# Kernel tuning notes

Measured on AMD Instinct MI355X. Metric: run time of the kernel, lower is better.

Reference implementation:

```python
import jax, jax.numpy as jnp
import numpy as np

B, L, M = 2, 1024, 32
F_DIM, C_DIM = 256, 32
H, QK = 12, 16
INF = 100000.0
EPS_DIR = 1e-4
LN_EPS = 1e-5
BETA_COEF = float(np.sqrt(2.0 / 9.0) / 2.0)
LOGIT_SCALE = float(np.sqrt(1.0 / 3.0))


def gather_nodes(a, nb):
    # a: (B,L,...,D), nb: (B,L,M) -> (B,L,M,...,D); row m of query l is node nb[b,l,m]
    return jax.vmap(lambda ab, nbb: ab[nbb])(a, nb)


def gather_pairs(z, nb):
    # z: (B,L,L,C), nb: (B,L,M) -> (B,L,M,C)
    idx = jnp.broadcast_to(nb[..., None], nb.shape + (z.shape[-1],))
    return jnp.take_along_axis(z, idx, axis=2)


def setup_inputs() -> dict:
    key = jax.random.key(0)
    ks = jax.random.split(key, 12)
    inp = {
        'R': jax.random.normal(ks[0], (B, L, 3, 3), jnp.float32),
        't': jax.random.normal(ks[1], (B, L, 3), jnp.float32),
        'p_CB': jax.random.normal(ks[2], (B, L, 3), jnp.float32),
        'x': jax.random.normal(ks[3], (B, L, F_DIM), jnp.float32),
        'z': jax.random.normal(ks[4], (B, L, L, C_DIM), jnp.float32),
        'mask': jnp.ones((B, L), dtype=bool),
        'neighbors': jax.random.randint(ks[5], (B, L, M), 0, L),
        'Wq': jax.random.normal(ks[6], (F_DIM, H * QK), jnp.float32) * 0.05,
        'Wk': jax.random.normal(ks[7], (F_DIM, H * QK), jnp.float32) * 0.05,
        'Wv': jax.random.normal(ks[8], (F_DIM, H * QK), jnp.float32) * 0.05,
        'Wpair': jax.random.normal(ks[9], (C_DIM, H), jnp.float32) * 0.1,
        'spatial_coef': jnp.full((1, 1, 1, H), float(np.log(np.e - 1.0)), jnp.float32),
        'Wout': jax.random.normal(ks[10], (H * C_DIM + H * QK + 7 * H, F_DIM), jnp.float32) * 0.05,
        'b_out': jnp.zeros((F_DIM,), jnp.float32),
        'ln_gamma': jnp.ones((F_DIM,), jnp.float32),
        'ln_beta': jnp.zeros((F_DIM,), jnp.float32),
    }
    return inp


def reference(R, t, p_CB, x, z, mask, neighbors, Wq, Wk, Wv, Wpair,
              spatial_coef, Wout, b_out, ln_gamma, ln_beta):
    Bn, Ln, Fn = x.shape
    # pair features of each query's KNN neighbors
    z_knn = gather_pairs(z, neighbors)                      # (B,L,M,C)
    # node logits
    q = (x @ Wq).reshape(Bn, Ln, H, QK)
    k = (x @ Wk).reshape(Bn, Ln, H, QK)
    k_knn = gather_nodes(k, neighbors)                      # (B,L,M,H,QK)
    logits_node = jnp.einsum('blhd,blmhd->blmh', q, k_knn)
    # pair bias logits
    logits_pair = z_knn @ Wpair                             # (B,L,M,H)
    # spatial (beta-carbon distance) logits; identical across heads before gamma
    p_knn = gather_nodes(p_CB, neighbors)                   # (B,L,M,3)
    d2 = jnp.sum((p_CB[:, :, None, :] - p_knn) ** 2, axis=-1)  # (B,L,M)
    gamma = jax.nn.softplus(spatial_coef)                   # (1,1,1,H)
    logits_spatial = d2[..., None] * (-gamma * BETA_COEF)   # (B,L,M,H)
    logits = (logits_node + logits_pair + logits_spatial) * LOGIT_SCALE
    # row-mask + softmax over neighbor dim
    mask_row = mask[:, :, None, None]                       # (B,L,1,1)
    logits = jnp.where(mask_row, logits, logits - INF)
    alpha = jax.nn.softmax(logits, axis=2)
    alpha = jnp.where(mask_row, alpha, jnp.zeros_like(alpha))
    # aggregations
    feat_p2n = jnp.einsum('blmh,blmc->blhc', alpha, z_knn).reshape(Bn, Ln, -1)
    v = (x @ Wv).reshape(Bn, Ln, H, QK)
    v_knn = gather_nodes(v, neighbors)                      # (B,L,M,H,QK)
    feat_node = jnp.einsum('blmh,blmhd->blhd', alpha, v_knn).reshape(Bn, Ln, -1)
    aggr = jnp.einsum('blmh,blmi->blhi', alpha, p_knn)      # (B,L,H,3) global coords
    # global_to_local: R^T (q - t)
    local = jnp.einsum('blji,blhj->blhi', R, aggr - t[:, :, None, :])
    dist = jnp.linalg.norm(local, axis=-1)                  # (B,L,H)
    dirn = local / (jnp.linalg.norm(local, axis=-1, keepdims=True) + EPS_DIR)
    feat_spatial = jnp.concatenate([local.reshape(Bn, Ln, -1), dist,
                                    dirn.reshape(Bn, Ln, -1)], axis=-1)
    feat = jnp.concatenate([feat_p2n, feat_node, feat_spatial], axis=-1)
    out = feat @ Wout + b_out
    out = jnp.where(mask[:, :, None], out, jnp.zeros_like(out))
    h = x + out
    mu = jnp.mean(h, axis=-1, keepdims=True)
    var = jnp.var(h, axis=-1, keepdims=True)
    return (h - mu) / jnp.sqrt(var + LN_EPS) * ln_gamma + ln_beta
```

## Files before the change

### kernel.cpp

```cpp
#include <hip/hip_runtime.h>
#include <math.h>

#define B_   2
#define L_   1024
#define M_   32
#define F_   256
#define C_   32
#define H_   12
#define QK_  16
#define HQK  192
#define KV2  384
#define QKV3 576
#define FEAT 660
#define FPAD 672
#define A2S  1360
#define NTOK 2048

constexpr float EPS_DIR     = 1e-4f;
constexpr float LN_EPS      = 1e-5f;
constexpr float BETA_COEF   = 0.23570226039551585f;
constexpr float LOGIT_SCALE = 0.5773502691896258f;

typedef __attribute__((ext_vector_type(8))) short  bf16x8;
typedef __attribute__((ext_vector_type(4))) float  f32x4;
typedef __attribute__((ext_vector_type(8))) ushort u16x8;

static __device__ __forceinline__ ushort f2bf(float v) {
  union { float f; unsigned u; } x; x.f = v;
  unsigned r = x.u + 0x7FFFu + ((x.u >> 16) & 1u);
  return (ushort)(r >> 16);
}
static __device__ __forceinline__ float bf2f(ushort h) {
  union { float f; unsigned u; } x; x.u = ((unsigned)h) << 16;
  return x.f;
}
static __device__ __forceinline__ void split4(const float* v,
                                              ushort4& h, ushort4& l) {
  h.x = f2bf(v[0]); l.x = f2bf(v[0] - bf2f(h.x));
  h.y = f2bf(v[1]); l.y = f2bf(v[1] - bf2f(h.y));
  h.z = f2bf(v[2]); l.z = f2bf(v[2] - bf2f(h.z));
  h.w = f2bf(v[3]); l.w = f2bf(v[3] - bf2f(h.w));
}
static __device__ __forceinline__ ushort4 pack4(const float* v) {
  ushort4 h;
  h.x = f2bf(v[0]); h.y = f2bf(v[1]);
  h.z = f2bf(v[2]); h.w = f2bf(v[3]);
  return h;
}
static __device__ __forceinline__ void wave_sync() {
  asm volatile("s_waitcnt lgkmcnt(0)" ::: "memory");
}

__global__ __launch_bounds__(256) void qkv_prep_kernel(
    const float* __restrict__ x,
    const float* __restrict__ Wq, const float* __restrict__ Wk,
    const float* __restrict__ Wv, const float* __restrict__ Wout,
    const float* __restrict__ z, const int* __restrict__ neighbors,
    float* __restrict__ qf, ushort* __restrict__ kvb,
    ushort* __restrict__ wo,
    ushort* __restrict__ z_d) {
  __shared__ ushort Ah[64][36], Al[64][36];
  __shared__ ushort Bh[64][36];
  const int bx  = blockIdx.x;
  const int tid = threadIdx.x;

  if (bx < 512) {
    const int t0 = bx * 4;
    for (int i = tid; i < 1024; i += 256) {
      int t = i >> 8, r = i & 255, m = r >> 3, cq = r & 7;
      int tok = t0 + t;
      int nb  = neighbors[tok * M_ + m];
      float4 v = *(const float4*)&z[((size_t)tok * L_ + nb) * C_ + cq * 4];
      *(ushort4*)&z_d[((size_t)tok * M_ + m) * C_ + cq * 4] =
          pack4((const float*)&v);
    }
    return;
  }
  if (bx < 544) {
    const int base = (bx - 512) * 256 + tid;
#pragma unroll
    for (int rep = 0; rep < 6; ++rep) {
      int qid = base + rep * 8192;
      if (qid < 43008) {
        int col = qid / 168;
        int k   = (qid - col * 168) * 4;
        float v[4];
#pragma unroll
        for (int j = 0; j < 4; ++j)
          v[j] = (k + j < FEAT) ? Wout[(size_t)(k + j) * F_ + col] : 0.f;
        ushort4 h4 = pack4(v);
        int off = (k >> 5) * 32 + ((k & 16) >> 4) * 4 + ((k & 12) << 1);
        *(ushort4*)&wo[(size_t)col * FPAD + off] = h4;
      }
    }
    return;
  }

  const int bxm = bx - 544;
  const int t0  = (bxm & 31) * 64;
  const int c0  = (bxm >> 5) * 64;
  const int w   = tid >> 6;
  const int l   = tid & 63;
  const int lr  = l & 15;
  const int lk  = (l >> 4) * 4;

  const float* Wb   = (c0 < HQK) ? Wq : (c0 < 2 * HQK) ? Wk : Wv;
  const int    cOff = (c0 < HQK) ? c0 : (c0 < 2 * HQK) ? c0 - HQK
                                                       : c0 - 2 * HQK;

  union ABFrag { bf16x8 v; ushort4 h[2]; };

  const int arow0 = tid >> 3,  akc0 = (tid & 7) * 4;
  const int arow1 = (tid + 256) >> 3, akc1 = ((tid + 256) & 7) * 4;
  const int bk0 = tid >> 4,  bcc0 = (tid & 15) * 4;
  const int bk1 = (tid + 256) >> 4, bcc1 = ((tid + 256) & 15) * 4;

  f32x4 acc[4];
#pragma unroll
  for (int n = 0; n < 4; ++n) acc[n] = (f32x4){0.f, 0.f, 0.f, 0.f};

  float4 xr0 = *(const float4*)&x[(size_t)(t0 + arow0) * F_ + akc0];
  float4 xr1 = *(const float4*)&x[(size_t)(t0 + arow1) * F_ + akc1];
  float4 wr0 = *(const float4*)&Wb[(size_t)bk0 * HQK + cOff + bcc0];
  float4 wr1 = *(const float4*)&Wb[(size_t)bk1 * HQK + cOff + bcc1];

  for (int s = 0; s < 8; ++s) {
    __syncthreads();
    {
      ushort4 h4, l4;
      split4((const float*)&xr0, h4, l4);
      *(ushort4*)&Ah[arow0][akc0] = h4;
      *(ushort4*)&Al[arow0][akc0] = l4;
      split4((const float*)&xr1, h4, l4);
      *(ushort4*)&Ah[arow1][akc1] = h4;
      *(ushort4*)&Al[arow1][akc1] = l4;
      ushort4 b0 = pack4((const float*)&wr0);
      Bh[bcc0 + 0][bk0] = b0.x;  Bh[bcc0 + 1][bk0] = b0.y;
      Bh[bcc0 + 2][bk0] = b0.z;  Bh[bcc0 + 3][bk0] = b0.w;
      ushort4 b1 = pack4((const float*)&wr1);
      Bh[bcc1 + 0][bk1] = b1.x;  Bh[bcc1 + 1][bk1] = b1.y;
      Bh[bcc1 + 2][bk1] = b1.z;  Bh[bcc1 + 3][bk1] = b1.w;
    }
    __syncthreads();

    if (s < 7) {
      int sn = (s + 1) * 32;
      xr0 = *(const float4*)&x[(size_t)(t0 + arow0) * F_ + sn + akc0];
      xr1 = *(const float4*)&x[(size_t)(t0 + arow1) * F_ + sn + akc1];
      wr0 = *(const float4*)&Wb[(size_t)(sn + bk0) * HQK + cOff + bcc0];
      wr1 = *(const float4*)&Wb[(size_t)(sn + bk1) * HQK + cOff + bcc1];
    }

    ABFrag a_h, a_l;
    a_h.h[0] = *(const ushort4*)&Ah[w * 16 + lr][lk];
    a_h.h[1] = *(const ushort4*)&Ah[w * 16 + lr][16 + lk];
    a_l.h[0] = *(const ushort4*)&Al[w * 16 + lr][lk];
    a_l.h[1] = *(const ushort4*)&Al[w * 16 + lr][16 + lk];
#pragma unroll
    for (int n = 0; n < 4; ++n) {
      ABFrag b_h;
      b_h.h[0] = *(const ushort4*)&Bh[n * 16 + lr][lk];
      b_h.h[1] = *(const ushort4*)&Bh[n * 16 + lr][16 + lk];
      acc[n] = __builtin_amdgcn_mfma_f32_16x16x32_bf16(a_h.v, b_h.v, acc[n], 0, 0, 0);
      acc[n] = __builtin_amdgcn_mfma_f32_16x16x32_bf16(a_l.v, b_h.v, acc[n], 0, 0, 0);
    }
  }

  if (c0 < HQK) {
#pragma unroll
    for (int n = 0; n < 4; ++n)
#pragma unroll
      for (int i = 0; i < 4; ++i)
        qf[(size_t)(t0 + w * 16 + lk + i) * HQK + c0 + n * 16 + lr] =
            acc[n][i];
  } else {
    const int cb0 = c0 - HQK;
#pragma unroll
    for (int n = 0; n < 4; ++n)
#pragma unroll
      for (int i = 0; i < 4; ++i)
        kvb[(size_t)(t0 + w * 16 + lk + i) * KV2 + cb0 + n * 16 + lr] =
            f2bf(acc[n][i]);
  }
}

__global__ __launch_bounds__(512) void attn_out_kernel(
    const float* __restrict__ R, const float* __restrict__ tvec,
    const float* __restrict__ pCB, const ushort* __restrict__ z_d,
    const int*   __restrict__ neighbors,
    const float* __restrict__ Wpair, const float* __restrict__ spatial_coef,
    const float* __restrict__ qf, const ushort* __restrict__ kvb,
    const ushort* __restrict__ wo,
    const float* __restrict__ b_out, const float* __restrict__ x,
    const float* __restrict__ ln_g, const float* __restrict__ ln_b,
    float* __restrict__ out) {
  const int tid   = threadIdx.x;
  const int t0    = blockIdx.x * 8;
  const int bbase = t0 & ~(L_ - 1);

  __shared__ float  q_s[8][HQK];
  __shared__ ushort z_s[8][M_][36];
  __shared__ float  alpha_s[8][M_][13];
  __shared__ float  p_s[8][M_][4];
  __shared__ float  wp_s[C_ * H_];
  __shared__ float  gam_s[H_];
  __shared__ float  geo_s[8][16];
  __shared__ int    nb_s[8][M_];
  __shared__ float  aggr_s[8][H_][4];
  __shared__ ushort A2[8][A2S];
  __shared__ float  part[16][8][2];
  __shared__ float  mu_s[16], rs_s[16];

  if (tid < 256) {
    int t = tid >> 5, m = tid & 31;
    nb_s[t][m] = neighbors[(t0 + t) * M_ + m];
  } else if (tid - 256 < H_) {
    gam_s[tid - 256] = log1pf(expf(spatial_coef[tid - 256]));
  }
  if (tid < C_ * H_) wp_s[tid] = Wpair[tid];
  if (tid < 96) {
    int t = tid / 12, c = FEAT + tid % 12;
    A2[t][(c >> 2) * 8 + (c & 3)]     = 0;
    A2[t][(c >> 2) * 8 + (c & 3) + 4] = 0;
  }
  if (tid < 384) {
    int t = tid / 48, r = tid % 48;
    *(float4*)&q_s[t][r * 4] =
        *(const float4*)&qf[(size_t)(t0 + t) * HQK + r * 4];
  }
  if (tid >= 384 && tid < 504) {
    int j = tid - 384, t = j / 15, w = j % 15;
    geo_s[t][w] = (w < 3) ? pCB[(t0 + t) * 3 + w]
                : (w < 6) ? tvec[(t0 + t) * 3 + (w - 3)]
                          : R[(t0 + t) * 9 + (w - 6)];
  }
  for (int i = tid; i < 2048; i += 512) {
    int t = i >> 8, r = i & 255, m = r >> 3, cq = r & 7;
    ushort4 v = *(const ushort4*)&z_d[((size_t)(t0 + t) * M_ + m) * C_ + cq * 4];
    *(ushort4*)&z_s[t][m][cq * 4] = v;
  }
  for (int i = tid; i < 8 * M_ * 3; i += 512) {
    int t = i / 96, r = i % 96, m = r / 3, ii = r % 3;
    int nb = neighbors[(t0 + t) * M_ + m];
    p_s[t][m][ii] = pCB[(bbase + nb) * 3 + ii];
  }
  __syncthreads();

  const int wv = tid >> 6;
  const int l  = tid & 63;

  {
    const int t  = wv;
    const int m  = l & 31;
    const int hb = (l >> 5) * 6;
    const int nb = nb_s[t][m];
    float lg[6];
#pragma unroll
    for (int h = 0; h < 6; ++h) lg[h] = 0.f;
#pragma unroll
    for (int c = 0; c < C_; ++c) {
      float zv = bf2f(z_s[t][m][c]);
#pragma unroll
      for (int h = 0; h < 6; ++h) lg[h] += zv * wp_s[c * H_ + hb + h];
    }
    union U8 { u16x8 v; ushort e[8]; };
    const ushort* kr = kvb + (size_t)(bbase + nb) * KV2;
#pragma unroll
    for (int h = 0; h < 6; ++h) {
      const int hh = hb + h;
      U8 ka, kb2;
      ka.v  = *(const u16x8*)&kr[hh * 16];
      kb2.v = *(const u16x8*)&kr[hh * 16 + 8];
      const float4* q4 = (const float4*)&q_s[t][hh * 16];
      float4 qa = q4[0], qb = q4[1], qc = q4[2], qd = q4[3];
      float nd = bf2f(ka.e[0]) * qa.x + bf2f(ka.e[1]) * qa.y
               + bf2f(ka.e[2]) * qa.z + bf2f(ka.e[3]) * qa.w
               + bf2f(ka.e[4]) * qb.x + bf2f(ka.e[5]) * qb.y
               + bf2f(ka.e[6]) * qb.z + bf2f(ka.e[7]) * qb.w
               + bf2f(kb2.e[0]) * qc.x + bf2f(kb2.e[1]) * qc.y
               + bf2f(kb2.e[2]) * qc.z + bf2f(kb2.e[3]) * qc.w
               + bf2f(kb2.e[4]) * qd.x + bf2f(kb2.e[5]) * qd.y
               + bf2f(kb2.e[6]) * qd.z + bf2f(kb2.e[7]) * qd.w;
      lg[h] += nd;
    }
    float dx = geo_s[t][0] - p_s[t][m][0];
    float dy = geo_s[t][1] - p_s[t][m][1];
    float dz = geo_s[t][2] - p_s[t][m][2];
    float d2 = dx * dx + dy * dy + dz * dz;
#pragma unroll
    for (int h = 0; h < 6; ++h)
      lg[h] = (lg[h] - d2 * gam_s[hb + h] * BETA_COEF) * LOGIT_SCALE;
#pragma unroll
    for (int h = 0; h < 6; ++h) {
      float mx = lg[h];
#pragma unroll
      for (int o = 16; o; o >>= 1) mx = fmaxf(mx, __shfl_xor(mx, o));
      float p = expf(lg[h] - mx);
      float s = p;
#pragma unroll
      for (int o = 16; o; o >>= 1) s += __shfl_xor(s, o);
      alpha_s[t][m][hb + h] = p / s;
    }
  }
  wave_sync();

  {
    const int t = wv;
    const int hp = l >> 3, cq = l & 7;
    if (hp < 6) {
      float acc0[4] = {0, 0, 0, 0}, acc1[4] = {0, 0, 0, 0};
#pragma unroll
      for (int m = 0; m < M_; ++m) {
        float a0 = alpha_s[t][m][hp * 2];
        float a1 = alpha_s[t][m][hp * 2 + 1];
        ushort4 zz = *(const ushort4*)&z_s[t][m][cq * 4];
        float z0 = bf2f(zz.x), z1 = bf2f(zz.y);
        float z2 = bf2f(zz.z), z3 = bf2f(zz.w);
        acc0[0] += a0 * z0; acc0[1] += a0 * z1;
        acc0[2] += a0 * z2; acc0[3] += a0 * z3;
        acc1[0] += a1 * z0; acc1[1] += a1 * z1;
        acc1[2] += a1 * z2; acc1[3] += a1 * z3;
      }
      ushort4 h4, l4;
      int c = (hp * 2) * C_ + cq * 4;
      split4(acc0, h4, l4);
      *(ushort4*)&A2[t][c * 2]     = h4;
      *(ushort4*)&A2[t][c * 2 + 4] = l4;
      c = (hp * 2 + 1) * C_ + cq * 4;
      split4(acc1, h4, l4);
      *(ushort4*)&A2[t][c * 2]     = h4;
      *(ushort4*)&A2[t][c * 2 + 4] = l4;
    }
  }
  {
    const int t = wv;
    const int h = l >> 2, dq = l & 3;
    if (h < 12) {
      float acc[4] = {0, 0, 0, 0};
#pragma unroll
      for (int m = 0; m < M_; ++m) {
        float a = alpha_s[t][m][h];
        const ushort* vr = kvb + (size_t)(bbase + nb_s[t][m]) * KV2 + HQK;
        ushort4 v4 = *(const ushort4*)&vr[h * QK_ + dq * 4];
        acc[0] += a * bf2f(v4.x); acc[1] += a * bf2f(v4.y);
        acc[2] += a * bf2f(v4.z); acc[3] += a * bf2f(v4.w);
      }
      ushort4 h4, l4;
      split4(acc, h4, l4);
      int c = 384 + h * QK_ + dq * 4;
      *(ushort4*)&A2[t][c * 2]     = h4;
      *(ushort4*)&A2[t][c * 2 + 4] = l4;
    }
  }
  if (l < 36) {
    const int t = wv;
    int h = l / 3, ii = l % 3;
    float f = 0.f;
#pragma unroll
    for (int m = 0; m < M_; ++m) f += alpha_s[t][m][h] * p_s[t][m][ii];
    aggr_s[t][h][ii] = f;
  }
  wave_sync();

  if (l < 12) {
    const int t = wv;
    const int h = l;
    float a0 = aggr_s[t][h][0] - geo_s[t][3];
    float a1 = aggr_s[t][h][1] - geo_s[t][4];
    float a2 = aggr_s[t][h][2] - geo_s[t][5];
    float lx = geo_s[t][6] * a0 + geo_s[t][9]  * a1 + geo_s[t][12] * a2;
    float ly = geo_s[t][7] * a0 + geo_s[t][10] * a1 + geo_s[t][13] * a2;
    float lz = geo_s[t][8] * a0 + geo_s[t][11] * a1 + geo_s[t][14] * a2;
    float dist = sqrtf(lx * lx + ly * ly + lz * lz);
    float inv  = 1.f / (dist + EPS_DIR);
    float vals[7] = {lx, ly, lz, dist, lx * inv, ly * inv, lz * inv};
    int   cols[7] = {576 + 3 * h, 577 + 3 * h, 578 + 3 * h, 612 + h,
                     624 + 3 * h, 625 + 3 * h, 626 + 3 * h};
#pragma unroll
    for (int j = 0; j < 7; ++j) {
      int c = cols[j];
      ushort hh = f2bf(vals[j]);
      A2[t][(c >> 2) * 8 + (c & 3)]     = hh;
      A2[t][(c >> 2) * 8 + (c & 3) + 4] = f2bf(vals[j] - bf2f(hh));
    }
  }

  const int w  = wv;
  const int lr = l & 15, lk = (l >> 4) * 4;
  const int atok = lr & 7;
  const int asel = (lr >> 3) * 4;
  const int col0 = (w * 2 + 0) * 16 + lr;
  const int col1 = (w * 2 + 1) * 16 + lr;
  const ushort* wo0 = wo + (size_t)col0 * FPAD + lk * 2;
  const ushort* wo1 = wo + (size_t)col1 * FPAD + lk * 2;

  union ABFrag { bf16x8 v; ushort4 h[2]; };
  union B8 { u16x8 v; ushort4 q[2]; };

  B8 pb[4][2];

#define PREF_B(sstep, buf) do {                                          \
    pb[buf][0].v = *(const u16x8*)&wo0[(sstep) * 32];                    \
    pb[buf][1].v = *(const u16x8*)&wo1[(sstep) * 32];                    \
  } while (0)

  PREF_B(0, 0);
  PREF_B(1, 1);
  PREF_B(2, 2);
  PREF_B(3, 3);
  __syncthreads();

  f32x4 acc[2];
  acc[0] = (f32x4){0.f, 0.f, 0.f, 0.f};
  acc[1] = (f32x4){0.f, 0.f, 0.f, 0.f};

#pragma unroll
  for (int s = 0; s < 21; ++s) {
    const int cb = s & 3;
    const int k0 = s * 32 + lk;
    ABFrag a;
    a.h[0] = *(const ushort4*)&A2[atok][k0 * 2 + asel];
    a.h[1] = *(const ushort4*)&A2[atok][(k0 + 16) * 2 + asel];
    ABFrag b0, b1;
    b0.h[0] = pb[cb][0].q[0];  b0.h[1] = pb[cb][0].q[1];
    b1.h[0] = pb[cb][1].q[0];  b1.h[1] = pb[cb][1].q[1];
    if (s < 17) PREF_B(s + 4, cb);
    acc[0] = __builtin_amdgcn_mfma_f32_16x16x32_bf16(a.v, b0.v, acc[0], 0, 0, 0);
    acc[1] = __builtin_amdgcn_mfma_f32_16x16x32_bf16(a.v, b1.v, acc[1], 0, 0, 0);
  }
#undef PREF_B

#pragma unroll
  for (int n = 0; n < 2; ++n)
#pragma unroll
    for (int i = 0; i < 4; ++i)
      acc[n][i] += __shfl_xor(acc[n][i], 32);

  float hv[4][2];
#pragma unroll
  for (int i = 0; i < 4; ++i) {
    const int row = (lk + i) & 7;
#pragma unroll
    for (int n = 0; n < 2; ++n) {
      const int col = (w * 2 + n) * 16 + lr;
      hv[i][n] = acc[n][i] + b_out[col] + x[(size_t)(t0 + row) * F_ + col];
    }
  }
#pragma unroll
  for (int i = 0; i < 4; ++i) {
    float s  = hv[i][0] + hv[i][1];
    float sq = hv[i][0] * hv[i][0] + hv[i][1] * hv[i][1];
#pragma unroll
    for (int o = 1; o < 16; o <<= 1) {
      s  += __shfl_xor(s, o);
      sq += __shfl_xor(sq, o);
    }
    if (lr == 0) {
      part[lk + i][w][0] = s;
      part[lk + i][w][1] = sq;
    }
  }
  __syncthreads();
  if (tid < 16) {
    float s = 0.f, sq = 0.f;
#pragma unroll
    for (int ww = 0; ww < 8; ++ww) {
      s  += part[tid][ww][0];
      sq += part[tid][ww][1];
    }
    float mu = s * (1.f / F_);
    mu_s[tid] = mu;
    rs_s[tid] = rsqrtf(sq * (1.f / F_) - mu * mu + LN_EPS);
  }
  __syncthreads();

  if (lk < 8) {
#pragma unroll
    for (int n = 0; n < 2; ++n) {
      const int col = (w * 2 + n) * 16 + lr;
      const float g = ln_g[col], be = ln_b[col];
#pragma unroll
      for (int i = 0; i < 4; ++i) {
        const int row = lk + i;
        out[(size_t)(t0 + row) * F_ + col] =
            (hv[i][n] - mu_s[row]) * rs_s[row] * g + be;
      }
    }
  }
}

extern "C" void kernel_launch(void* const* d_in, const int* in_sizes, int n_in,
                              void* d_out, int out_size, void* d_ws,
                              size_t ws_size, hipStream_t stream) {
  const float* R     = (const float*)d_in[0];
  const float* t     = (const float*)d_in[1];
  const float* pCB   = (const float*)d_in[2];
  const float* x     = (const float*)d_in[3];
  const float* z     = (const float*)d_in[4];
  const int*   nb    = (const int*)d_in[6];
  const float* Wq    = (const float*)d_in[7];
  const float* Wk    = (const float*)d_in[8];
  const float* Wv    = (const float*)d_in[9];
  const float* Wpair = (const float*)d_in[10];
  const float* sc    = (const float*)d_in[11];
  const float* Wout  = (const float*)d_in[12];
  const float* bout  = (const float*)d_in[13];
  const float* g     = (const float*)d_in[14];
  const float* be    = (const float*)d_in[15];
  float* out  = (float*)d_out;

  float*  qf   = (float*)d_ws;
  ushort* kvb  = (ushort*)(qf + (size_t)NTOK * HQK);
  ushort* z_d  = kvb + (size_t)NTOK * KV2;
  ushort* wo   = z_d + (size_t)NTOK * M_ * C_;

  qkv_prep_kernel<<<832, 256, 0, stream>>>(x, Wq, Wk, Wv, Wout, z, nb,
                                           qf, kvb, wo, z_d);
  attn_out_kernel<<<NTOK / 8, 512, 0, stream>>>(R, t, pCB, z_d, nb, Wpair,
                                                sc, qf, kvb, wo, bout, x,
                                                g, be, out);
}
```

Before: 37.58 us.

## Halve attn_out block to 256 threads with two tokens and four column tiles per wave

The attention/output kernel drops from 8 waves to 4 waves per block. Each wave now handles two tokens in the softmax and aggregation phases, and four 16-column output tiles in the MFMA projection. The prefetch depth for Wout drops from 4 stages to 2, while each stage loads four fragments. The intent is to reuse each A fragment across more MFMAs and to cut per-block synchronisation and launch cost. The trade-offs are higher register pressure, more serial work per wave and lower latency hiding.

Measured after the change: 47.07 us. +25.3%, slower.

```diff
diff --git a/kernel.cpp b/kernel.cpp
--- a/kernel.cpp
+++ b/kernel.cpp
@@ -184,7 +184,7 @@
   }
 }
 
-__global__ __launch_bounds__(512) void attn_out_kernel(
+__global__ __launch_bounds__(256) void attn_out_kernel(
     const float* __restrict__ R, const float* __restrict__ tvec,
     const float* __restrict__ pCB, const ushort* __restrict__ z_d,
     const int*   __restrict__ neighbors,
@@ -208,38 +208,37 @@
   __shared__ int    nb_s[8][M_];
   __shared__ float  aggr_s[8][H_][4];
   __shared__ ushort A2[8][A2S];
-  __shared__ float  part[16][8][2];
+  __shared__ float  part[16][4][2];
   __shared__ float  mu_s[16], rs_s[16];
 
-  if (tid < 256) {
+  {
     int t = tid >> 5, m = tid & 31;
     nb_s[t][m] = neighbors[(t0 + t) * M_ + m];
-  } else if (tid - 256 < H_) {
-    gam_s[tid - 256] = log1pf(expf(spatial_coef[tid - 256]));
-  }
-  if (tid < C_ * H_) wp_s[tid] = Wpair[tid];
+  }
+  if (tid < H_) gam_s[tid] = log1pf(expf(spatial_coef[tid]));
+  for (int i = tid; i < C_ * H_; i += 256) wp_s[i] = Wpair[i];
   if (tid < 96) {
     int t = tid / 12, c = FEAT + tid % 12;
     A2[t][(c >> 2) * 8 + (c & 3)]     = 0;
     A2[t][(c >> 2) * 8 + (c & 3) + 4] = 0;
   }
-  if (tid < 384) {
-    int t = tid / 48, r = tid % 48;
+  for (int i = tid; i < 384; i += 256) {
+    int t = i / 48, r = i % 48;
     *(float4*)&q_s[t][r * 4] =
         *(const float4*)&qf[(size_t)(t0 + t) * HQK + r * 4];
   }
-  if (tid >= 384 && tid < 504) {
-    int j = tid - 384, t = j / 15, w = j % 15;
+  if (tid >= 128 && tid < 248) {
+    int j = tid - 128, t = j / 15, w = j % 15;
     geo_s[t][w] = (w < 3) ? pCB[(t0 + t) * 3 + w]
                 : (w < 6) ? tvec[(t0 + t) * 3 + (w - 3)]
                           : R[(t0 + t) * 9 + (w - 6)];
   }
-  for (int i = tid; i < 2048; i += 512) {
+  for (int i = tid; i < 2048; i += 256) {
     int t = i >> 8, r = i & 255, m = r >> 3, cq = r & 7;
     ushort4 v = *(const ushort4*)&z_d[((size_t)(t0 + t) * M_ + m) * C_ + cq * 4];
     *(ushort4*)&z_s[t][m][cq * 4] = v;
   }
-  for (int i = tid; i < 8 * M_ * 3; i += 512) {
+  for (int i = tid; i < 8 * M_ * 3; i += 256) {
     int t = i / 96, r = i % 96, m = r / 3, ii = r % 3;
     int nb = neighbors[(t0 + t) * M_ + m];
     p_s[t][m][ii] = pCB[(bbase + nb) * 3 + ii];
@@ -249,8 +248,8 @@
   const int wv = tid >> 6;
   const int l  = tid & 63;
 
-  {
-    const int t  = wv;
+  for (int tt = 0; tt < 2; ++tt) {
+    const int t  = wv * 2 + tt;
     const int m  = l & 31;
     const int hb = (l >> 5) * 6;
     const int nb = nb_s[t][m];
@@ -304,8 +303,8 @@
   }
   wave_sync();
 
-  {
-    const int t = wv;
+  for (int tt = 0; tt < 2; ++tt) {
+    const int t = wv * 2 + tt;
     const int hp = l >> 3, cq = l & 7;
     if (hp < 6) {
       float acc0[4] = {0, 0, 0, 0}, acc1[4] = {0, 0, 0, 0};
@@ -332,8 +331,8 @@
       *(ushort4*)&A2[t][c * 2 + 4] = l4;
     }
   }
-  {
-    const int t = wv;
+  for (int tt = 0; tt < 2; ++tt) {
+    const int t = wv * 2 + tt;
     const int h = l >> 2, dq = l & 3;
     if (h < 12) {
       float acc[4] = {0, 0, 0, 0};
@@ -352,119 +351,130 @@
       *(ushort4*)&A2[t][c * 2 + 4] = l4;
     }
   }
-  if (l < 36) {
-    const int t = wv;
-    int h = l / 3, ii = l % 3;
-    float f = 0.f;
-#pragma unroll
-    for (int m = 0; m < M_; ++m) f += alpha_s[t][m][h] * p_s[t][m][ii];
-    aggr_s[t][h][ii] = f;
+  for (int tt = 0; tt < 2; ++tt) {
+    const int t = wv * 2 + tt;
+    if (l < 36) {
+      int h = l / 3, ii = l % 3;
+      float f = 0.f;
+#pragma unroll
+      for (int m = 0; m < M_; ++m) f += alpha_s[t][m][h] * p_s[t][m][ii];
+      aggr_s[t][h][ii] = f;
+    }
   }
   wave_sync();
 
-  if (l < 12) {
-    const int t = wv;
-    const int h = l;
-    float a0 = aggr_s[t][h][0] - geo_s[t][3];
-    float a1 = aggr_s[t][h][1] - geo_s[t][4];
-    float a2 = aggr_s[t][h][2] - geo_s[t][5];
-    float lx = geo_s[t][6] * a0 + geo_s[t][9]  * a1 + geo_s[t][12] * a2;
-    float ly = geo_s[t][7] * a0 + geo_s[t][10] * a1 + geo_s[t][13] * a2;
-    float lz = geo_s[t][8] * a0 + geo_s[t][11] * a1 + geo_s[t][14] * a2;
-    float dist = sqrtf(lx * lx + ly * ly + lz * lz);
-    float inv  = 1.f / (dist + EPS_DIR);
-    float vals[7] = {lx, ly, lz, dist, lx * inv, ly * inv, lz * inv};
-    int   cols[7] = {576 + 3 * h, 577 + 3 * h, 578 + 3 * h, 612 + h,
-                     624 + 3 * h, 625 + 3 * h, 626 + 3 * h};
-#pragma unroll
-    for (int j = 0; j < 7; ++j) {
-      int c = cols[j];
-      ushort hh = f2bf(vals[j]);
-      A2[t][(c >> 2) * 8 + (c & 3)]     = hh;
-      A2[t][(c >> 2) * 8 + (c & 3) + 4] = f2bf(vals[j] - bf2f(hh));
-    }
-  }
-
-  const int w  = wv;
+  for (int tt = 0; tt < 2; ++tt) {
+    const int t = wv * 2 + tt;
+    if (l < 12) {
+      const int h = l;
+      float a0 = aggr_s[t][h][0] - geo_s[t][3];
+      float a1 = aggr_s[t][h][1] - geo_s[t][4];
+      float a2 = aggr_s[t][h][2] - geo_s[t][5];
+      float lx = geo_s[t][6] * a0 + geo_s[t][9]  * a1 + geo_s[t][12] * a2;
+      float ly = geo_s[t][7] * a0 + geo_s[t][10] * a1 + geo_s[t][13] * a2;
+      float lz = geo_s[t][8] * a0 + geo_s[t][11] * a1 + geo_s[t][14] * a2;
+      float dist = sqrtf(lx * lx + ly * ly + lz * lz);
+      float inv  = 1.f / (dist + EPS_DIR);
+      float vals[7] = {lx, ly, lz, dist, lx * inv, ly * inv, lz * inv};
+      int   cols[7] = {576 + 3 * h, 577 + 3 * h, 578 + 3 * h, 612 + h,
+                       624 + 3 * h, 625 + 3 * h, 626 + 3 * h};
+#pragma unroll
+      for (int j = 0; j < 7; ++j) {
+        int c = cols[j];
+        ushort hh = f2bf(vals[j]);
+        A2[t][(c >> 2) * 8 + (c & 3)]     = hh;
+        A2[t][(c >> 2) * 8 + (c & 3) + 4] = f2bf(vals[j] - bf2f(hh));
+      }
+    }
+  }
+
   const int lr = l & 15, lk = (l >> 4) * 4;
   const int atok = lr & 7;
   const int asel = (lr >> 3) * 4;
-  const int col0 = (w * 2 + 0) * 16 + lr;
-  const int col1 = (w * 2 + 1) * 16 + lr;
-  const ushort* wo0 = wo + (size_t)col0 * FPAD + lk * 2;
-  const ushort* wo1 = wo + (size_t)col1 * FPAD + lk * 2;
+  int colv[4];
+  const ushort* wop[4];
+#pragma unroll
+  for (int n = 0; n < 4; ++n) {
+    colv[n] = (wv * 4 + n) * 16 + lr;
+    wop[n]  = wo + (size_t)colv[n] * FPAD + lk * 2;
+  }
 
   union ABFrag { bf16x8 v; ushort4 h[2]; };
   union B8 { u16x8 v; ushort4 q[2]; };
 
-  B8 pb[4][2];
+  B8 pb[2][4];
 
 #define PREF_B(sstep, buf) do {                                          \
-    pb[buf][0].v = *(const u16x8*)&wo0[(sstep) * 32];                    \
-    pb[buf][1].v = *(const u16x8*)&wo1[(sstep) * 32];                    \
+    pb[buf][0].v = *(const u16x8*)&wop[0][(sstep) * 32];                 \
+    pb[buf][1].v = *(const u16x8*)&wop[1][(sstep) * 32];                 \
+    pb[buf][2].v = *(const u16x8*)&wop[2][(sstep) * 32];                 \
+    pb[buf][3].v = *(const u16x8*)&wop[3][(sstep) * 32];                 \
   } while (0)
 
   PREF_B(0, 0);
   PREF_B(1, 1);
-  PREF_B(2, 2);
-  PREF_B(3, 3);
   __syncthreads();
 
-  f32x4 acc[2];
-  acc[0] = (f32x4){0.f, 0.f, 0.f, 0.f};
-  acc[1] = (f32x4){0.f, 0.f, 0.f, 0.f};
+  f32x4 acc[4];
+#pragma unroll
+  for (int n = 0; n < 4; ++n) acc[n] = (f32x4){0.f, 0.f, 0.f, 0.f};
 
 #pragma unroll
   for (int s = 0; s < 21; ++s) {
-    const int cb = s & 3;
+    const int cb = s & 1;
     const int k0 = s * 32 + lk;
     ABFrag a;
     a.h[0] = *(const ushort4*)&A2[atok][k0 * 2 + asel];
     a.h[1] = *(const ushort4*)&A2[atok][(k0 + 16) * 2 + asel];
-    ABFrag b0, b1;
-    b0.h[0] = pb[cb][0].q[0];  b0.h[1] = pb[cb][0].q[1];
-    b1.h[0] = pb[cb][1].q[0];  b1.h[1] = pb[cb][1].q[1];
-    if (s < 17) PREF_B(s + 4, cb);
-    acc[0] = __builtin_amdgcn_mfma_f32_16x16x32_bf16(a.v, b0.v, acc[0], 0, 0, 0);
-    acc[1] = __builtin_amdgcn_mfma_f32_16x16x32_bf16(a.v, b1.v, acc[1], 0, 0, 0);
+    ABFrag b[4];
+#pragma unroll
+    for (int n = 0; n < 4; ++n) {
+      b[n].h[0] = pb[cb][n].q[0];
+      b[n].h[1] = pb[cb][n].q[1];
+    }
+    if (s < 19) PREF_B(s + 2, cb);
+    acc[0] = __builtin_amdgcn_mfma_f32_16x16x32_bf16(a.v, b[0].v, acc[0], 0, 0, 0);
+    acc[1] = __builtin_amdgcn_mfma_f32_16x16x32_bf16(a.v, b[1].v, acc[1], 0, 0, 0);
+    acc[2] = __builtin_amdgcn_mfma_f32_16x16x32_bf16(a.v, b[2].v, acc[2], 0, 0, 0);
+    acc[3] = __builtin_amdgcn_mfma_f32_16x16x32_bf16(a.v, b[3].v, acc[3], 0, 0, 0);
   }
 #undef PREF_B
 
 #pragma unroll
-  for (int n = 0; n < 2; ++n)
+  for (int n = 0; n < 4; ++n)
 #pragma unroll
     for (int i = 0; i < 4; ++i)
       acc[n][i] += __shfl_xor(acc[n][i], 32);
 
-  float hv[4][2];
+  float hv[4][4];
 #pragma unroll
   for (int i = 0; i < 4; ++i) {
     const int row = (lk + i) & 7;
 #pragma unroll
-    for (int n = 0; n < 2; ++n) {
-      const int col = (w * 2 + n) * 16 + lr;
-      hv[i][n] = acc[n][i] + b_out[col] + x[(size_t)(t0 + row) * F_ + col];
-    }
+    for (int n = 0; n < 4; ++n)
+      hv[i][n] = acc[n][i] + b_out[colv[n]] +
+                 x[(size_t)(t0 + row) * F_ + colv[n]];
   }
 #pragma unroll
   for (int i = 0; i < 4; ++i) {
-    float s  = hv[i][0] + hv[i][1];
-    float sq = hv[i][0] * hv[i][0] + hv[i][1] * hv[i][1];
+    float s  = hv[i][0] + hv[i][1] + hv[i][2] + hv[i][3];
+    float sq = hv[i][0] * hv[i][0] + hv[i][1] * hv[i][1] +
+               hv[i][2] * hv[i][2] + hv[i][3] * hv[i][3];
 #pragma unroll
     for (int o = 1; o < 16; o <<= 1) {
       s  += __shfl_xor(s, o);
       sq += __shfl_xor(sq, o);
     }
     if (lr == 0) {
-      part[lk + i][w][0] = s;
-      part[lk + i][w][1] = sq;
+      part[lk + i][wv][0] = s;
+      part[lk + i][wv][1] = sq;
     }
   }
   __syncthreads();
   if (tid < 16) {
     float s = 0.f, sq = 0.f;
 #pragma unroll
-    for (int ww = 0; ww < 8; ++ww) {
+    for (int ww = 0; ww < 4; ++ww) {
       s  += part[tid][ww][0];
       sq += part[tid][ww][1];
     }
@@ -476,8 +486,8 @@
 
   if (lk < 8) {
 #pragma unroll
-    for (int n = 0; n < 2; ++n) {
-      const int col = (w * 2 + n) * 16 + lr;
+    for (int n = 0; n < 4; ++n) {
+      const int col = colv[n];
       const float g = ln_g[col], be = ln_b[col];
 #pragma unroll
       for (int i = 0; i < 4; ++i) {
@@ -516,7 +526,7 @@
 
   qkv_prep_kernel<<<832, 256, 0, stream>>>(x, Wq, Wk, Wv, Wout, z, nb,
                                            qf, kvb, wo, z_d);
-  attn_out_kernel<<<NTOK / 8, 512, 0, stream>>>(R, t, pCB, z_d, nb, Wpair,
+  attn_out_kernel<<<NTOK / 8, 256, 0, stream>>>(R, t, pCB, z_d, nb, Wpair,
                                                 sc, qf, kvb, wo, bout, x,
                                                 g, be, out);
 }
```
